# Optimization experiments

Hardware: AMD Instinct MI355X
Metric: run time of the kernel (lower is better)

## Reference

```python
import jax, jax.numpy as jnp
import numpy as np

CHANNELS = 256
NUM_HEADS = 4
GROUPS = 8
EPS = 1e-5


def setup_inputs() -> dict:
    key = jax.random.key(0)
    ks = jax.random.split(key, 5)
    C = CHANNELS
    x = jax.random.normal(ks[0], (2, C, 16, 16, 16), dtype=jnp.float32)
    # GroupNorm affine params
    norm_w = jnp.ones((C,), dtype=jnp.float32)
    norm_b = jnp.zeros((C,), dtype=jnp.float32)
    # 1x1x1 Conv3d weights collapsed to dense matrices [out, in]
    fan = 1.0 / np.sqrt(C)
    qkv_w = jax.random.uniform(ks[1], (3 * C, C), jnp.float32, -fan, fan)
    qkv_b = jax.random.uniform(ks[2], (3 * C,), jnp.float32, -fan, fan)
    proj_w = jax.random.uniform(ks[3], (C, C), jnp.float32, -fan, fan)
    proj_b = jax.random.uniform(ks[4], (C,), jnp.float32, -fan, fan)
    return {"x": x, "norm_w": norm_w, "norm_b": norm_b,
            "qkv_w": qkv_w, "qkv_b": qkv_b,
            "proj_w": proj_w, "proj_b": proj_b}


def _group_norm(x, w, b):
    B, C, D, H, W = x.shape
    xg = x.reshape(B, GROUPS, C // GROUPS, D, H, W)
    mean = xg.mean(axis=(2, 3, 4, 5), keepdims=True)
    var = xg.var(axis=(2, 3, 4, 5), keepdims=True)
    xn = (xg - mean) * jax.lax.rsqrt(var + EPS)
    xn = xn.reshape(B, C, D, H, W)
    return xn * w[None, :, None, None, None] + b[None, :, None, None, None]


def reference(x, norm_w, norm_b, qkv_w, qkv_b, proj_w, proj_b):
    B, C, D, H, W = x.shape
    N = D * H * W
    hd = C // NUM_HEADS
    h = _group_norm(x, norm_w, norm_b)
    # 1x1x1 conv == channel matmul: [B, 3C, N]
    hf = h.reshape(B, C, N)
    qkv = jnp.einsum('oc,bcn->bon', qkv_w, hf) + qkv_b[None, :, None]
    q, k, v = jnp.split(qkv, 3, axis=1)
    q = q.reshape(B, NUM_HEADS, hd, N)
    k = k.reshape(B, NUM_HEADS, hd, N)
    v = v.reshape(B, NUM_HEADS, hd, N)
    scale = hd ** (-0.5)
    attn = jax.nn.softmax(jnp.einsum('bhcn,bhcm->bhnm', q, k) * scale, axis=-1)
    o = jnp.einsum('bhnm,bhcm->bhcn', attn, v)  # [B, H, hd, N]
    o = o.reshape(B, C, N)
    o = jnp.einsum('oc,bcn->bon', proj_w, o) + proj_b[None, :, None]
    return x + o.reshape(B, C, D, H, W)
```

## Files before the change

kernel.cpp:

```cpp
#include <hip/hip_runtime.h>
#include <hip/hip_bf16.h>

#define BATCH 2
#define CH 256
#define NH 4
#define HD 64
#define NGROUP 8
#define CPG 32
#define NTOK 4096
#define EPSV 1e-5f
#define QSCALE 0.1803368801111204f
#define NSPLIT 4

typedef __attribute__((ext_vector_type(8))) short short8;
typedef __attribute__((ext_vector_type(4))) short s4bf;
typedef __attribute__((ext_vector_type(4))) float float4v;

__device__ __forceinline__ unsigned short f2bf(float f) {
    union { float f; unsigned u; } v; v.f = f;
    unsigned r = v.u + 0x7FFF + ((v.u >> 16) & 1);
    return (unsigned short)(r >> 16);
}
__device__ __forceinline__ unsigned short f2bf_fast(float f) {
    union { float f; unsigned u; } v; v.f = f;
    return (unsigned short)((v.u + 0x8000u) >> 16);
}
__device__ __forceinline__ float bf2f(unsigned short u) {
    union { unsigned u; float f; } v; v.u = ((unsigned)u) << 16;
    return v.f;
}
__device__ __forceinline__ unsigned pk2bf(float a, float b) {
#if __has_builtin(__builtin_amdgcn_cvt_pk_bf16_f32)
    typedef __attribute__((ext_vector_type(2))) __bf16 bf2v;
    bf2v p = __builtin_amdgcn_cvt_pk_bf16_f32(a, b);
    union { bf2v v; unsigned u; } c; c.v = p;
    return c.u;
#else
    return (unsigned)f2bf_fast(a) | ((unsigned)f2bf_fast(b) << 16);
#endif
}

__global__ void prep(const float* __restrict__ x,
                     const float* __restrict__ qkv_w, const float* __restrict__ qkv_b,
                     const float* __restrict__ proj_w,
                     float* __restrict__ psum, float* __restrict__ psq,
                     unsigned short* __restrict__ wq, float* __restrict__ bq,
                     unsigned short* __restrict__ wp) {
    int bx = blockIdx.x;
    int t = threadIdx.x;
    if (bx < 256) {
        int s = bx & 15, g = (bx >> 4) & 7, b = bx >> 7;
        const float* base = x + ((size_t)(b * CH + g * CPG)) * NTOK + (size_t)s * 8192;
        float sum = 0.f, sq = 0.f;
        const float4v* p4 = (const float4v*)base;
        for (int i = 0; i < 8; ++i) {
            float4v v = p4[t + i * 256];
            for (int j = 0; j < 4; ++j) { sum += v[j]; sq += v[j] * v[j]; }
        }
        for (int off = 32; off; off >>= 1) {
            sum += __shfl_down(sum, off, 64);
            sq  += __shfl_down(sq,  off, 64);
        }
        __shared__ float ls[8];
        int wave = t >> 6, lane = t & 63;
        if (lane == 0) { ls[wave * 2] = sum; ls[wave * 2 + 1] = sq; }
        __syncthreads();
        if (t == 0) {
            float S = 0.f, Q = 0.f;
            for (int w = 0; w < 4; ++w) { S += ls[w * 2]; Q += ls[w * 2 + 1]; }
            int idx = (b * NGROUP + g) * 16 + s;
            psum[idx] = S; psq[idx] = Q;
        }
    } else {
        int idx = (bx - 256) * 256 + t;
        int stride = 256 * 256;
        for (int i = idx; i < 3 * CH * CH; i += stride) {
            float f = qkv_w[i];
            if (i < CH * CH) f *= QSCALE;
            wq[i] = f2bf(f);
        }
        for (int i = idx; i < CH * CH; i += stride) wp[i] = f2bf(proj_w[i]);
        for (int i = idx; i < 3 * CH; i += stride) {
            float f = qkv_b[i];
            if (i < CH) f *= QSCALE;
            bq[i] = f;
        }
    }
}

__global__ void gn_norm(const float* __restrict__ x, const float* __restrict__ nw,
                        const float* __restrict__ nb_, const float* __restrict__ psum,
                        const float* __restrict__ psq, unsigned short* __restrict__ hT) {
    int t = threadIdx.x;
    int n = blockIdx.x * 64 + (t & 63);
    int g = blockIdx.y;
    int cb = g * 32 + (t >> 6) * 8;
    int b = blockIdx.z;
    float S = 0.f, Q = 0.f;
    for (int s = 0; s < 16; ++s) {
        S += psum[(b * NGROUP + g) * 16 + s];
        Q += psq[(b * NGROUP + g) * 16 + s];
    }
    const float M = (float)(CPG * NTOK);
    float mean = S / M;
    float inv  = rsqrtf(Q / M - mean * mean + EPSV);
    short8 h8;
    for (int j = 0; j < 8; ++j) {
        int c = cb + j;
        float w  = nw[c] * inv;
        float bb = nb_[c] - mean * w;
        float v = x[((size_t)(b * CH + c)) * NTOK + n];
        h8[j] = (short)f2bf(v * w + bb);
    }
    *(short8*)(hT + ((size_t)b * NTOK + n) * CH + cb) = h8;
}

__global__ __launch_bounds__(256) void qkv_gemm(const unsigned short* __restrict__ hT,
        const unsigned short* __restrict__ wq, const float* __restrict__ bq,
        unsigned short* __restrict__ qT, unsigned short* __restrict__ kT,
        unsigned short* __restrict__ vv) {
    int nb = blockIdx.x;
    int ob = blockIdx.y;
    int b  = blockIdx.z;
    int t = threadIdx.x;
    int wave = t >> 6, lane = t & 63;
    int l15 = lane & 15, quad = lane >> 4;
    int o0 = ob * 64 + wave * 16;

    __shared__ __align__(16) unsigned short bt[64 * 264];

    short8 aW[8];
    {
        const unsigned short* wr = wq + (size_t)(o0 + l15) * CH + quad * 8;
        for (int kc = 0; kc < 8; ++kc) aW[kc] = *(const short8*)(wr + kc * 32);
    }
    for (int p = 0; p < 8; ++p) {
        int slot = p * 256 + t;
        int r = slot >> 5, c = slot & 31;
        *(short8*)(bt + r * 264 + c * 8) =
            *(const short8*)(hT + ((size_t)b * NTOK + nb * 64 + r) * CH + c * 8);
    }
    __syncthreads();

    float4v acc[4];
    for (int nt = 0; nt < 4; ++nt) for (int r = 0; r < 4; ++r) acc[nt][r] = 0.f;
    for (int kc = 0; kc < 8; ++kc) {
        for (int nt = 0; nt < 4; ++nt) {
            short8 pb = *(const short8*)(bt + (nt * 16 + l15) * 264 + kc * 32 + quad * 8);
            acc[nt] = __builtin_amdgcn_mfma_f32_16x16x32_bf16(aW[kc], pb, acc[nt], 0, 0, 0);
        }
    }
    for (int nt = 0; nt < 4; ++nt) {
        int n = nb * 64 + nt * 16 + l15;
        for (int r = 0; r < 4; ++r) {
            int o = o0 + quad * 4 + r;
            float val = acc[nt][r] + bq[o];
            unsigned short bv = f2bf(val);
            int cch = o & 255;
            int seg = o >> 8;
            int hh = cch >> 6, ci = cch & 63;
            if (seg == 0)      qT[(((size_t)b * NH + hh) * NTOK + n) * HD + ci] = bv;
            else if (seg == 1) kT[(((size_t)b * NH + hh) * NTOK + n) * HD + ci] = bv;
            else               vv[(((size_t)b * NH + hh) * HD + ci) * NTOK + n] = bv;
        }
    }
}

__global__ __launch_bounds__(256, 4) void attn_kernel(const unsigned short* __restrict__ qT,
        const unsigned short* __restrict__ kT, const unsigned short* __restrict__ vv,
        unsigned short* __restrict__ opb, float* __restrict__ lpb) {
    int nb = blockIdx.x;
    int h  = blockIdx.y;
    int zb = blockIdx.z;
    int sp = zb & 3, b = zb >> 2;
    int t = threadIdx.x, wave = t >> 6, lane = t & 63;
    int l15 = lane & 15, quad = lane >> 4;
    int n0 = nb * 128 + wave * 32;
    int kv0 = sp * (NTOK / NSPLIT);

    unsigned short* opart = opb + (size_t)sp * ((size_t)BATCH * NTOK * CH);
    float* lpart = lpb + (size_t)sp * (BATCH * NH * NTOK);

    const unsigned short* qbh = qT + ((size_t)(b * NH + h)) * NTOK * HD;
    const unsigned short* kbh = kT + ((size_t)(b * NH + h)) * NTOK * HD;
    const unsigned short* vbh = vv + ((size_t)(b * NH + h)) * HD * NTOK;

    __shared__ __align__(16) unsigned short kbuf[128 * 80];
    __shared__ __align__(16) unsigned short vbuf[64 * 136];

    short8 aQ[2][2];
    for (int mt = 0; mt < 2; ++mt) {
        aQ[mt][0] = *(const short8*)(qbh + (size_t)(n0 + mt * 16 + l15) * HD + quad * 8);
        aQ[mt][1] = *(const short8*)(qbh + (size_t)(n0 + mt * 16 + l15) * HD + 32 + quad * 8);
    }

    float l_p[2] = {0.f, 0.f};
    float4v o_acc[2][4];
    for (int mt = 0; mt < 2; ++mt)
        for (int ct = 0; ct < 4; ++ct)
            for (int r = 0; r < 4; ++r) o_acc[mt][ct][r] = 0.f;

    for (int ms = kv0; ms < kv0 + NTOK / NSPLIT; ms += 128) {
        __syncthreads();
#pragma unroll
        for (int p = 0; p < 4; ++p) {
            int slot = p * 256 + t;
            int r = slot >> 3, c = slot & 7;
            short8 kd = *(const short8*)(kbh + (size_t)(ms + r) * HD + c * 8);
            *(short8*)(kbuf + r * 80 + c * 8) = kd;
        }
#pragma unroll
        for (int p = 0; p < 4; ++p) {
            int slot = p * 256 + t;
            int r = slot >> 4, c = slot & 15;
            short8 vd = *(const short8*)(vbh + (size_t)r * NTOK + ms + c * 8);
            *(short8*)(vbuf + r * 136 + c * 8) = vd;
        }
        __syncthreads();

#pragma unroll
        for (int kh = 0; kh < 2; ++kh) {
            float4v s[2][4];
#pragma unroll
            for (int nt = 0; nt < 4; ++nt) {
                int krow = kh * 64 + nt * 16 + l15;
                short8 ak0 = *(const short8*)(kbuf + krow * 80 + quad * 8);
                short8 ak1 = *(const short8*)(kbuf + krow * 80 + 32 + quad * 8);
#pragma unroll
                for (int mt = 0; mt < 2; ++mt) {
                    float4v z;
                    for (int r = 0; r < 4; ++r) z[r] = 0.f;
                    z = __builtin_amdgcn_mfma_f32_16x16x32_bf16(ak0, aQ[mt][0], z, 0, 0, 0);
                    z = __builtin_amdgcn_mfma_f32_16x16x32_bf16(ak1, aQ[mt][1], z, 0, 0, 0);
                    s[mt][nt] = z;
                }
            }
            s4bf aP[2][4];
#pragma unroll
            for (int mt = 0; mt < 2; ++mt) {
#pragma unroll
                for (int nt = 0; nt < 4; ++nt) {
                    float e0 = __builtin_amdgcn_exp2f(s[mt][nt][0]);
                    float e1 = __builtin_amdgcn_exp2f(s[mt][nt][1]);
                    float e2 = __builtin_amdgcn_exp2f(s[mt][nt][2]);
                    float e3 = __builtin_amdgcn_exp2f(s[mt][nt][3]);
                    l_p[mt] += (e0 + e1) + (e2 + e3);
                    union { s4bf v; unsigned u[2]; } c;
                    c.u[0] = pk2bf(e0, e1);
                    c.u[1] = pk2bf(e2, e3);
                    aP[mt][nt] = c.v;
                }
            }
#pragma unroll
            for (int ct = 0; ct < 4; ++ct) {
#pragma unroll
                for (int nt = 0; nt < 4; ++nt) {
                    s4bf bv = *(const s4bf*)(vbuf + (ct * 16 + l15) * 136 + kh * 64 + nt * 16 + quad * 4);
#pragma unroll
                    for (int mt = 0; mt < 2; ++mt)
                        o_acc[mt][ct] = __builtin_amdgcn_mfma_f32_16x16x16bf16_1k(aP[mt][nt], bv, o_acc[mt][ct], 0, 0, 0);
                }
            }
        }
    }
    for (int mt = 0; mt < 2; ++mt) {
        l_p[mt] += __shfl_xor(l_p[mt], 16, 64);
        l_p[mt] += __shfl_xor(l_p[mt], 32, 64);
    }
    for (int mt = 0; mt < 2; ++mt) {
        for (int ct = 0; ct < 4; ++ct) {
            for (int r = 0; r < 4; ++r) {
                int n = n0 + mt * 16 + quad * 4 + r;
                int cg = h * HD + ct * 16 + l15;
                opart[((size_t)b * NTOK + n) * CH + cg] = f2bf(o_acc[mt][ct][r]);
            }
        }
        if (lane < 16)
            lpart[((size_t)(b * NH + h)) * NTOK + n0 + mt * 16 + lane] = l_p[mt];
    }
}

__global__ __launch_bounds__(256) void proj_gemm(const unsigned short* __restrict__ opb,
        const float* __restrict__ lpb, const unsigned short* __restrict__ wp,
        const float* __restrict__ proj_b, const float* __restrict__ x,
        float* __restrict__ out) {
    int nb = blockIdx.x;
    int cb = blockIdx.y;
    int b  = blockIdx.z;
    int t = threadIdx.x, wave = t >> 6, lane = t & 63;
    int l15 = lane & 15, quad = lane >> 4;
    int c0 = cb * 64 + wave * 16;
    const size_t OP = (size_t)BATCH * NTOK * CH;
    const size_t LP = (size_t)BATCH * NH * NTOK;

    __shared__ __align__(16) unsigned short bt[64 * 264];
    __shared__ float rl[64 * 4];

    short8 aW[8];
    {
        const unsigned short* wr = wp + (size_t)(c0 + l15) * CH + quad * 8;
        for (int kc = 0; kc < 8; ++kc) aW[kc] = *(const short8*)(wr + kc * 32);
    }
    {
        int r = t >> 2, h = t & 3;
        size_t lidx = ((size_t)(b * NH + h)) * NTOK + nb * 64 + r;
        float ls = (lpb[lidx] + lpb[LP + lidx]) + (lpb[2 * LP + lidx] + lpb[3 * LP + lidx]);
        rl[r * 4 + h] = 1.0f / ls;
    }
    __syncthreads();
    for (int p = 0; p < 8; ++p) {
        int slot = p * 256 + t;
        int r = slot >> 5, c = slot & 31;
        size_t base = ((size_t)b * NTOK + nb * 64 + r) * CH + c * 8;
        short8 o0 = *(const short8*)(opb + base);
        short8 o1 = *(const short8*)(opb + OP + base);
        short8 o2 = *(const short8*)(opb + 2 * OP + base);
        short8 o3 = *(const short8*)(opb + 3 * OP + base);
        float rinv = rl[r * 4 + (c >> 3)];
        short8 m;
        for (int j = 0; j < 8; ++j) {
            float f = (bf2f((unsigned short)o0[j]) + bf2f((unsigned short)o1[j]))
                    + (bf2f((unsigned short)o2[j]) + bf2f((unsigned short)o3[j]));
            m[j] = (short)f2bf(f * rinv);
        }
        *(short8*)(bt + r * 264 + c * 8) = m;
    }
    __syncthreads();

    float4v acc[4];
    for (int nt = 0; nt < 4; ++nt) for (int r = 0; r < 4; ++r) acc[nt][r] = 0.f;
    for (int kc = 0; kc < 8; ++kc) {
        for (int nt = 0; nt < 4; ++nt) {
            short8 pb = *(const short8*)(bt + (nt * 16 + l15) * 264 + kc * 32 + quad * 8);
            acc[nt] = __builtin_amdgcn_mfma_f32_16x16x32_bf16(aW[kc], pb, acc[nt], 0, 0, 0);
        }
    }
    for (int nt = 0; nt < 4; ++nt) {
        int n = nb * 64 + nt * 16 + l15;
        for (int r = 0; r < 4; ++r) {
            int cc = c0 + quad * 4 + r;
            size_t idx = ((size_t)(b * CH + cc)) * NTOK + n;
            out[idx] = acc[nt][r] + proj_b[cc] + x[idx];
        }
    }
}

extern "C" void kernel_launch(void* const* d_in, const int* in_sizes, int n_in,
                              void* d_out, int out_size, void* d_ws, size_t ws_size,
                              hipStream_t stream) {
    const float* x      = (const float*)d_in[0];
    const float* norm_w = (const float*)d_in[1];
    const float* norm_b = (const float*)d_in[2];
    const float* qkv_w  = (const float*)d_in[3];
    const float* qkv_b  = (const float*)d_in[4];
    const float* proj_w = (const float*)d_in[5];
    const float* proj_b = (const float*)d_in[6];
    float* out = (float*)d_out;

    char* ws = (char*)d_ws;
    float* psum  = (float*)ws;
    float* psq   = (float*)(ws + 1024);
    float* bqs   = (float*)(ws + 4096);
    unsigned short* wqb = (unsigned short*)(ws + 8192);
    unsigned short* wpb = (unsigned short*)(ws + 401408);
    float* lpb = (float*)(ws + 532480);
    const size_t MB4 = 4194304;
    unsigned short* hT  = (unsigned short*)(ws + 2097152);
    unsigned short* opb = hT;
    unsigned short* qT = (unsigned short*)(ws + 2097152 + 4 * MB4);
    unsigned short* kT = (unsigned short*)(ws + 2097152 + 5 * MB4);
    unsigned short* vv = (unsigned short*)(ws + 2097152 + 6 * MB4);

    prep<<<dim3(512), dim3(256), 0, stream>>>(x, qkv_w, qkv_b, proj_w, psum, psq, wqb, bqs, wpb);
    gn_norm<<<dim3(64, 8, BATCH), dim3(256), 0, stream>>>(x, norm_w, norm_b, psum, psq, hT);
    qkv_gemm<<<dim3(64, 12, BATCH), dim3(256), 0, stream>>>(hT, wqb, bqs, qT, kT, vv);
    attn_kernel<<<dim3(32, NH, BATCH * NSPLIT), dim3(256), 0, stream>>>(qT, kT, vv, opb, lpb);
    proj_gemm<<<dim3(64, 4, BATCH), dim3(256), 0, stream>>>(opb, lpb, wpb, proj_b, x, out);
}
```

Measured before the change: 154.9 us.

## Prefetch K/V tiles into registers, remap blocks across XCDs, vectorize QKV stores

```diff
diff --git a/kernel.cpp b/kernel.cpp
--- a/kernel.cpp
+++ b/kernel.cpp
@@ -150,18 +150,26 @@
             acc[nt] = __builtin_amdgcn_mfma_f32_16x16x32_bf16(aW[kc], pb, acc[nt], 0, 0, 0);
         }
     }
+    int seg = ob >> 2;
     for (int nt = 0; nt < 4; ++nt) {
         int n = nb * 64 + nt * 16 + l15;
-        for (int r = 0; r < 4; ++r) {
-            int o = o0 + quad * 4 + r;
-            float val = acc[nt][r] + bq[o];
-            unsigned short bv = f2bf(val);
-            int cch = o & 255;
-            int seg = o >> 8;
+        if (seg < 2) {
+            int ob_ = o0 + quad * 4;
+            int cch = ob_ & 255;
             int hh = cch >> 6, ci = cch & 63;
-            if (seg == 0)      qT[(((size_t)b * NH + hh) * NTOK + n) * HD + ci] = bv;
-            else if (seg == 1) kT[(((size_t)b * NH + hh) * NTOK + n) * HD + ci] = bv;
-            else               vv[(((size_t)b * NH + hh) * HD + ci) * NTOK + n] = bv;
+            s4bf pk;
+            for (int r = 0; r < 4; ++r)
+                pk[r] = (short)f2bf(acc[nt][r] + bq[ob_ + r]);
+            unsigned short* dst = (seg == 0) ? qT : kT;
+            *(s4bf*)(dst + (((size_t)b * NH + hh) * NTOK + n) * HD + ci) = pk;
+        } else {
+            for (int r = 0; r < 4; ++r) {
+                int o = o0 + quad * 4 + r;
+                float val = acc[nt][r] + bq[o];
+                int cch = o & 255;
+                int hh = cch >> 6, ci = cch & 63;
+                vv[(((size_t)b * NH + hh) * HD + ci) * NTOK + n] = f2bf(val);
+            }
         }
     }
 }
@@ -169,9 +177,12 @@
 __global__ __launch_bounds__(256, 4) void attn_kernel(const unsigned short* __restrict__ qT,
         const unsigned short* __restrict__ kT, const unsigned short* __restrict__ vv,
         unsigned short* __restrict__ opb, float* __restrict__ lpb) {
-    int nb = blockIdx.x;
-    int h  = blockIdx.y;
-    int zb = blockIdx.z;
+    int f = blockIdx.x + 32 * blockIdx.y + 128 * blockIdx.z;
+    int xcd = f & 7, j = f >> 3;
+    int nb = j >> 2;
+    int g  = xcd + 8 * (j & 3);
+    int h  = g & 3;
+    int zb = g >> 2;
     int sp = zb & 3, b = zb >> 2;
     int t = threadIdx.x, wave = t >> 6, lane = t & 63;
     int l15 = lane & 15, quad = lane >> 4;
@@ -185,7 +196,7 @@
     const unsigned short* kbh = kT + ((size_t)(b * NH + h)) * NTOK * HD;
     const unsigned short* vbh = vv + ((size_t)(b * NH + h)) * HD * NTOK;
 
-    __shared__ __align__(16) unsigned short kbuf[128 * 80];
+    __shared__ __align__(16) unsigned short kbuf[128 * 72];
     __shared__ __align__(16) unsigned short vbuf[64 * 136];
 
     short8 aQ[2][2];
@@ -200,32 +211,63 @@
         for (int ct = 0; ct < 4; ++ct)
             for (int r = 0; r < 4; ++r) o_acc[mt][ct][r] = 0.f;
 
-    for (int ms = kv0; ms < kv0 + NTOK / NSPLIT; ms += 128) {
-        __syncthreads();
+    short8 kreg[4], vreg[4];
+    {
+        int ms = kv0;
 #pragma unroll
         for (int p = 0; p < 4; ++p) {
             int slot = p * 256 + t;
             int r = slot >> 3, c = slot & 7;
-            short8 kd = *(const short8*)(kbh + (size_t)(ms + r) * HD + c * 8);
-            *(short8*)(kbuf + r * 80 + c * 8) = kd;
+            kreg[p] = *(const short8*)(kbh + (size_t)(ms + r) * HD + c * 8);
         }
 #pragma unroll
         for (int p = 0; p < 4; ++p) {
             int slot = p * 256 + t;
             int r = slot >> 4, c = slot & 15;
-            short8 vd = *(const short8*)(vbh + (size_t)r * NTOK + ms + c * 8);
-            *(short8*)(vbuf + r * 136 + c * 8) = vd;
-        }
+            vreg[p] = *(const short8*)(vbh + (size_t)r * NTOK + ms + c * 8);
+        }
+    }
+
+    for (int ms = kv0; ms < kv0 + NTOK / NSPLIT; ms += 128) {
         __syncthreads();
+#pragma unroll
+        for (int p = 0; p < 4; ++p) {
+            int slot = p * 256 + t;
+            int r = slot >> 3, c = slot & 7;
+            *(short8*)(kbuf + r * 72 + c * 8) = kreg[p];
+        }
+#pragma unroll
+        for (int p = 0; p < 4; ++p) {
+            int slot = p * 256 + t;
+            int r = slot >> 4, c = slot & 15;
+            *(short8*)(vbuf + r * 136 + c * 8) = vreg[p];
+        }
+        __syncthreads();
+        if (ms + 128 < kv0 + NTOK / NSPLIT) {
+            int mn = ms + 128;
+#pragma unroll
+            for (int p = 0; p < 4; ++p) {
+                int slot = p * 256 + t;
+                int r = slot >> 3, c = slot & 7;
+                kreg[p] = *(const short8*)(kbh + (size_t)(mn + r) * HD + c * 8);
+            }
+#pragma unroll
+            for (int p = 0; p < 4; ++p) {
+                int slot = p * 256 + t;
+                int r = slot >> 4, c = slot & 15;
+                vreg[p] = *(const short8*)(vbh + (size_t)r * NTOK + mn + c * 8);
+            }
+        }
 
 #pragma unroll
         for (int kh = 0; kh < 2; ++kh) {
             float4v s[2][4];
+            __builtin_amdgcn_s_setprio(1);
 #pragma unroll
             for (int nt = 0; nt < 4; ++nt) {
                 int krow = kh * 64 + nt * 16 + l15;
-                short8 ak0 = *(const short8*)(kbuf + krow * 80 + quad * 8);
-                short8 ak1 = *(const short8*)(kbuf + krow * 80 + 32 + quad * 8);
+                short8 ak0 = *(const short8*)(kbuf + krow * 72 + quad * 8);
+                short8 ak1 = *(const short8*)(kbuf + krow * 72 + 32 + quad * 8);
 #pragma unroll
                 for (int mt = 0; mt < 2; ++mt) {
                     float4v z;
@@ -235,6 +277,7 @@
                     s[mt][nt] = z;
                 }
             }
+            __builtin_amdgcn_s_setprio(0);
             s4bf aP[2][4];
 #pragma unroll
             for (int mt = 0; mt < 2; ++mt) {
@@ -251,6 +294,7 @@
                     aP[mt][nt] = c.v;
                 }
             }
+            __builtin_amdgcn_s_setprio(1);
 #pragma unroll
             for (int ct = 0; ct < 4; ++ct) {
 #pragma unroll
@@ -261,6 +305,7 @@
                         o_acc[mt][ct] = __builtin_amdgcn_mfma_f32_16x16x16bf16_1k(aP[mt][nt], bv, o_acc[mt][ct], 0, 0, 0);
                 }
             }
+            __builtin_amdgcn_s_setprio(0);
         }
     }
     for (int mt = 0; mt < 2; ++mt) {
```

Result: slower. 212.7 us (+37.3%).
